# Performance work log

Hardware: AMD Instinct MI355X
Metric: run time of the kernel (lower is better)

## Reference

```python
import jax, jax.numpy as jnp
import numpy as np

IN_FEATURES = 1024
OUT_FEATURES = 64
KERNEL_DIMS = 16
N = 512


def setup_inputs() -> dict:
    key = jax.random.key(0)
    kx, kT = jax.random.split(key)
    x = jax.random.normal(kx, (N, IN_FEATURES), dtype=jnp.float32)
    T = jax.random.normal(kT, (IN_FEATURES, OUT_FEATURES, KERNEL_DIMS), dtype=jnp.float32)
    return {"x": x, "T": T}


def reference(x, T):
    n = x.shape[0]
    # Project: [N, in] @ [in, out*kd] -> [N, out, kd]
    matrices = (x @ T.reshape(T.shape[0], -1)).reshape(n, OUT_FEATURES, KERNEL_DIMS)
    # Pairwise L1 distance over kernel dims: [N, N, out]
    norm = jnp.abs(matrices[None, :, :, :] - matrices[:, None, :, :]).sum(axis=3)
    expnorm = jnp.exp(-norm)
    # Exclude self-similarity (diagonal) and sum over the batch axis
    mask = 1.0 - jnp.eye(n, dtype=x.dtype)
    o_b = (expnorm * mask[:, :, None]).sum(axis=1)  # [N, out]
    return jnp.concatenate([x, o_b], axis=1)
```

## Files before the change

### kernel.cpp

```cpp
#include <hip/hip_runtime.h>
#include <hip/hip_bf16.h>
#include <hip/hip_fp16.h>

#define NB     512
#define INF    1024
#define OUTF   64
#define PROJ   1024
#define OROW   (INF + OUTF)

typedef short short8 __attribute__((ext_vector_type(8)));
typedef float floatx4 __attribute__((ext_vector_type(4)));

#define LDT 40

__device__ __forceinline__ unsigned pack_bf16(float x, float y) {
    __hip_bfloat162 h = __float22bfloat162_rn(make_float2(x, y));
    union { __hip_bfloat162 h; unsigned u; } v; v.h = h; return v.u;
}

__device__ __forceinline__ __half2 as_h2(unsigned u) {
    union { unsigned u; __half2 h; } v; v.u = u; return v.h;
}

__global__ __launch_bounds__(256, 2) void gemm_fused(const float* __restrict__ A,
                                                     const float* __restrict__ B,
                                                     float* __restrict__ out,
                                                     __half* __restrict__ M16) {
    __shared__ short As[16 * LDT];
    __shared__ short Bs[64 * LDT];

    const int t    = threadIdx.x;
    const int lane = t & 63, w = t >> 6;
    const int bnx = blockIdx.x, bmy = blockIdx.y;
    const int bm = bmy * 16, bn = bnx * 64;

    {
        const int r = t >> 4, c4 = (t & 15) * 4;
        *(float4*)&out[(size_t)(bm + r) * OROW + bn + c4] =
            *(const float4*)&A[(size_t)(bm + r) * INF + bn + c4];
    }
    if (t < 16) {
        const int row = bmy * 16 + bnx;
        *(float4*)&out[(size_t)row * OROW + INF + t * 4] =
            make_float4(-1.f, -1.f, -1.f, -1.f);
    }

    const int am = t >> 4,        ak  = (t & 15) * 2;
    const int bk = (t >> 4) * 2,  bn0 = (t & 15) * 4;

    const int q = lane >> 4, c = lane & 15;
    const short* ap = &As[c * LDT + q * 8];
    const short* bp = &Bs[(w * 16 + c) * LDT + q * 8];

    floatx4 acc = {0.f, 0.f, 0.f, 0.f};

    float2 av  = *(const float2*)&A[(size_t)(bm + am) * INF + ak];
    float4 bv0 = *(const float4*)&B[(size_t)bk * PROJ + bn + bn0];
    float4 bv1 = *(const float4*)&B[(size_t)(bk + 1) * PROJ + bn + bn0];

    for (int k0 = 0; k0 < INF; k0 += 32) {
        __syncthreads();
        *(unsigned*)&As[am * LDT + ak]        = pack_bf16(av.x, av.y);
        *(unsigned*)&Bs[(bn0 + 0) * LDT + bk] = pack_bf16(bv0.x, bv1.x);
        *(unsigned*)&Bs[(bn0 + 1) * LDT + bk] = pack_bf16(bv0.y, bv1.y);
        *(unsigned*)&Bs[(bn0 + 2) * LDT + bk] = pack_bf16(bv0.z, bv1.z);
        *(unsigned*)&Bs[(bn0 + 3) * LDT + bk] = pack_bf16(bv0.w, bv1.w);
        __syncthreads();

        const int kn = k0 + 32;
        if (kn < INF) {
            av  = *(const float2*)&A[(size_t)(bm + am) * INF + kn + ak];
            bv0 = *(const float4*)&B[(size_t)(kn + bk) * PROJ + bn + bn0];
            bv1 = *(const float4*)&B[(size_t)(kn + bk + 1) * PROJ + bn + bn0];
        }

        const short8 af = *(const short8*)ap;
        const short8 bf = *(const short8*)bp;
        acc = __builtin_amdgcn_mfma_f32_16x16x32_bf16(af, bf, acc, 0, 0, 0);
    }

#pragma unroll
    for (int r = 0; r < 4; ++r) {
        M16[(size_t)(bm + q * 4 + r) * PROJ + bn + w * 16 + c] = __float2half(acc[r]);
    }
}

__global__ __launch_bounds__(128) void pairwise_h2(const __half* __restrict__ M16,
                                                   float* __restrict__ out) {
    __shared__ __half Mj[64 * 64];

    const int t  = threadIdx.x;
    const int o  = t & 3;
    const int il = t >> 2;
    const int og = blockIdx.x;
    const int ig = blockIdx.y;
    const int j0 = blockIdx.z * 64;
    const int i  = ig * 32 + il;

    const uint4* mp = (const uint4*)&M16[(size_t)i * PROJ + og * 64 + o * 16];
    const uint4 a0 = mp[0], a1 = mp[1];

#pragma unroll
    for (int cc = 0; cc < 4; ++cc) {
        const int idx = (cc * 128 + t) * 8;
        const int jl  = idx >> 6;
        const int col = idx & 63;
        *(uint4*)&Mj[jl * 64 + col] =
            *(const uint4*)&M16[(size_t)(j0 + jl) * PROJ + og * 64 + col];
    }
    __syncthreads();

    float sum0 = 0.f, sum1 = 0.f;
#pragma unroll 4
    for (int jl = 0; jl < 64; ++jl) {
        const uint4 b0 = *(const uint4*)&Mj[jl * 64 + o * 16];
        const uint4 b1 = *(const uint4*)&Mj[jl * 64 + o * 16 + 8];
        __half2 s0 = __hadd2(__habs2(__hsub2(as_h2(a0.x), as_h2(b0.x))),
                             __habs2(__hsub2(as_h2(a0.y), as_h2(b0.y))));
        __half2 s1 = __hadd2(__habs2(__hsub2(as_h2(a0.z), as_h2(b0.z))),
                             __habs2(__hsub2(as_h2(a0.w), as_h2(b0.w))));
        __half2 s2 = __hadd2(__habs2(__hsub2(as_h2(a1.x), as_h2(b1.x))),
                             __habs2(__hsub2(as_h2(a1.y), as_h2(b1.y))));
        __half2 s3 = __hadd2(__habs2(__hsub2(as_h2(a1.z), as_h2(b1.z))),
                             __habs2(__hsub2(as_h2(a1.w), as_h2(b1.w))));
        const __half2 s = __hadd2(__hadd2(s0, s1), __hadd2(s2, s3));
        const float norm = __low2float(s) + __high2float(s);
        if (jl & 1) sum1 += __expf(-norm);
        else        sum0 += __expf(-norm);
    }

    __hip_atomic_fetch_add(&out[(size_t)i * OROW + INF + og * 4 + o],
                           sum0 + sum1, __ATOMIC_RELAXED,
                           __HIP_MEMORY_SCOPE_AGENT);
}

extern "C" void kernel_launch(void* const* d_in, const int* in_sizes, int n_in,
                              void* d_out, int out_size, void* d_ws, size_t ws_size,
                              hipStream_t stream) {
    const float* x = (const float*)d_in[0];
    const float* T = (const float*)d_in[1];
    float* out  = (float*)d_out;
    __half* M16 = (__half*)d_ws;

    gemm_fused<<<dim3(PROJ / 64, NB / 16), 256, 0, stream>>>(x, T, out, M16);
    pairwise_h2<<<dim3(OUTF / 4, NB / 32, NB / 64), 128, 0, stream>>>(M16, out);
}
```

Measured before the change: 92.56 us.

## Double GEMM K-step with k-major B tile and reuse Mj across two rows

The GEMM now stages 64 K values per iteration in a new shared layout (A row-major and B k-pair-major as packed bf16 pairs) and issues two MFMAs per barrier pair. This halves the number of syncthreads and makes the global loads wider. The pairwise kernel gives each thread two i rows, so every Mj tile read from shared memory feeds two L1-distance computations and the grid's y dimension is halved. This raises register use and lowers block count, which could hurt occupancy and latency hiding.

Result: faster. 88.94 us (-3.9%).

```diff
diff --git a/kernel.cpp b/kernel.cpp
--- a/kernel.cpp
+++ b/kernel.cpp
@@ -11,7 +11,8 @@
 typedef short short8 __attribute__((ext_vector_type(8)));
 typedef float floatx4 __attribute__((ext_vector_type(4)));
 
-#define LDT 40
+#define SA 36
+#define SB 68
 
 __device__ __forceinline__ unsigned pack_bf16(float x, float y) {
     __hip_bfloat162 h = __float22bfloat162_rn(make_float2(x, y));
@@ -26,8 +27,8 @@
                                                      const float* __restrict__ B,
                                                      float* __restrict__ out,
                                                      __half* __restrict__ M16) {
-    __shared__ short As[16 * LDT];
-    __shared__ short Bs[64 * LDT];
+    __shared__ unsigned As[16 * SA];
+    __shared__ unsigned Bs[32 * SB];
 
     const int t    = threadIdx.x;
     const int lane = t & 63, w = t >> 6;
@@ -45,44 +46,78 @@
             make_float4(-1.f, -1.f, -1.f, -1.f);
     }
 
-    const int am = t >> 4,        ak  = (t & 15) * 2;
-    const int bk = (t >> 4) * 2,  bn0 = (t & 15) * 4;
+    const int am  = t >> 4;
+    const int ak  = (t & 15) * 4;
+    const int bkp = t >> 4;
+    const int bn0 = (t & 15) * 4;
 
     const int q = lane >> 4, c = lane & 15;
-    const short* ap = &As[c * LDT + q * 8];
-    const short* bp = &Bs[(w * 16 + c) * LDT + q * 8];
+    const unsigned* apo = &As[c * SA + q * 4];
+    const unsigned* bpo = &Bs[(q * 4) * SB + w * 16 + c];
 
     floatx4 acc = {0.f, 0.f, 0.f, 0.f};
 
-    float2 av  = *(const float2*)&A[(size_t)(bm + am) * INF + ak];
-    float4 bv0 = *(const float4*)&B[(size_t)bk * PROJ + bn + bn0];
-    float4 bv1 = *(const float4*)&B[(size_t)(bk + 1) * PROJ + bn + bn0];
+    const size_t aoff  = (size_t)(bm + am) * INF + ak;
+    const float* Bbase = B + bn + bn0;
 
-    for (int k0 = 0; k0 < INF; k0 += 32) {
+    float4 av  = *(const float4*)&A[aoff];
+    float4 b0a = *(const float4*)&Bbase[(size_t)(2 * bkp)      * PROJ];
+    float4 b0b = *(const float4*)&Bbase[(size_t)(2 * bkp + 1)  * PROJ];
+    float4 b1a = *(const float4*)&Bbase[(size_t)(2 * bkp + 32) * PROJ];
+    float4 b1b = *(const float4*)&Bbase[(size_t)(2 * bkp + 33) * PROJ];
+
+    for (int k0 = 0; k0 < INF; k0 += 64) {
         __syncthreads();
-        *(unsigned*)&As[am * LDT + ak]        = pack_bf16(av.x, av.y);
-        *(unsigned*)&Bs[(bn0 + 0) * LDT + bk] = pack_bf16(bv0.x, bv1.x);
-        *(unsigned*)&Bs[(bn0 + 1) * LDT + bk] = pack_bf16(bv0.y, bv1.y);
-        *(unsigned*)&Bs[(bn0 + 2) * LDT + bk] = pack_bf16(bv0.z, bv1.z);
-        *(unsigned*)&Bs[(bn0 + 3) * LDT + bk] = pack_bf16(bv0.w, bv1.w);
+        *(uint2*)&As[am * SA + (ak >> 1)] =
+            make_uint2(pack_bf16(av.x, av.y), pack_bf16(av.z, av.w));
+        *(uint4*)&Bs[bkp * SB + bn0] =
+            make_uint4(pack_bf16(b0a.x, b0b.x), pack_bf16(b0a.y, b0b.y),
+                       pack_bf16(b0a.z, b0b.z), pack_bf16(b0a.w, b0b.w));
+        *(uint4*)&Bs[(bkp + 16) * SB + bn0] =
+            make_uint4(pack_bf16(b1a.x, b1b.x), pack_bf16(b1a.y, b1b.y),
+                       pack_bf16(b1a.z, b1b.z), pack_bf16(b1a.w, b1b.w));
         __syncthreads();
 
-        const int kn = k0 + 32;
+        const int kn = k0 + 64;
         if (kn < INF) {
-            av  = *(const float2*)&A[(size_t)(bm + am) * INF + kn + ak];
-            bv0 = *(const float4*)&B[(size_t)(kn + bk) * PROJ + bn + bn0];
-            bv1 = *(const float4*)&B[(size_t)(kn + bk + 1) * PROJ + bn + bn0];
+            av  = *(const float4*)&A[aoff + kn];
+            b0a = *(const float4*)&Bbase[(size_t)(kn + 2 * bkp)      * PROJ];
+            b0b = *(const float4*)&Bbase[(size_t)(kn + 2 * bkp + 1)  * PROJ];
+            b1a = *(const float4*)&Bbase[(size_t)(kn + 2 * bkp + 32) * PROJ];
+            b1b = *(const float4*)&Bbase[(size_t)(kn + 2 * bkp + 33) * PROJ];
         }
 
-        const short8 af = *(const short8*)ap;
-        const short8 bf = *(const short8*)bp;
-        acc = __builtin_amdgcn_mfma_f32_16x16x32_bf16(af, bf, acc, 0, 0, 0);
+        union { uint4 u; short8 s; } alo, ahi;
+        alo.u = *(const uint4*)(apo);
+        ahi.u = *(const uint4*)(apo + 16);
+        union { unsigned u[4]; short8 s; } blo, bhi;
+#pragma unroll
+        for (int j = 0; j < 4; ++j) {
+            blo.u[j] = bpo[j * SB];
+            bhi.u[j] = bpo[(j + 16) * SB];
+        }
+        acc = __builtin_amdgcn_mfma_f32_16x16x32_bf16(alo.s, blo.s, acc, 0, 0, 0);
+        acc = __builtin_amdgcn_mfma_f32_16x16x32_bf16(ahi.s, bhi.s, acc, 0, 0, 0);
     }
 
 #pragma unroll
     for (int r = 0; r < 4; ++r) {
         M16[(size_t)(bm + q * 4 + r) * PROJ + bn + w * 16 + c] = __float2half(acc[r]);
     }
+}
+
+__device__ __forceinline__ float l1norm16(const uint4 a0, const uint4 a1,
+                                          const uint4 b0, const uint4 b1) {
+    __half2 s0 = __hadd2(__habs2(__hsub2(as_h2(a0.x), as_h2(b0.x))),
+                         __habs2(__hsub2(as_h2(a0.y), as_h2(b0.y))));
+    __half2 s1 = __hadd2(__habs2(__hsub2(as_h2(a0.z), as_h2(b0.z))),
+                         __habs2(__hsub2(as_h2(a0.w), as_h2(b0.w))));
+    __half2 s2 = __hadd2(__habs2(__hsub2(as_h2(a1.x), as_h2(b1.x))),
+                         __habs2(__hsub2(as_h2(a1.y), as_h2(b1.y))));
+    __half2 s3 = __hadd2(__habs2(__hsub2(as_h2(a1.z), as_h2(b1.z))),
+                         __habs2(__hsub2(as_h2(a1.w), as_h2(b1.w))));
+    const __half2 s = __hadd2(__hadd2(s0, s1), __hadd2(s2, s3));
+    return __low2float(s) + __high2float(s);
 }
 
 __global__ __launch_bounds__(128) void pairwise_h2(const __half* __restrict__ M16,
@@ -95,10 +130,13 @@
     const int og = blockIdx.x;
     const int ig = blockIdx.y;
     const int j0 = blockIdx.z * 64;
-    const int i  = ig * 32 + il;
+    const int ia = ig * 64 + il;
+    const int ib = ia + 32;
 
-    const uint4* mp = (const uint4*)&M16[(size_t)i * PROJ + og * 64 + o * 16];
-    const uint4 a0 = mp[0], a1 = mp[1];
+    const uint4* mpa = (const uint4*)&M16[(size_t)ia * PROJ + og * 64 + o * 16];
+    const uint4* mpb = (const uint4*)&M16[(size_t)ib * PROJ + og * 64 + o * 16];
+    const uint4 a0 = mpa[0], a1 = mpa[1];
+    const uint4 a2 = mpb[0], a3 = mpb[1];
 
 #pragma unroll
     for (int cc = 0; cc < 4; ++cc) {
@@ -110,28 +148,21 @@
     }
     __syncthreads();
 
-    float sum0 = 0.f, sum1 = 0.f;
+    float sa0 = 0.f, sa1 = 0.f, sb0 = 0.f, sb1 = 0.f;
 #pragma unroll 4
     for (int jl = 0; jl < 64; ++jl) {
         const uint4 b0 = *(const uint4*)&Mj[jl * 64 + o * 16];
         const uint4 b1 = *(const uint4*)&Mj[jl * 64 + o * 16 + 8];
-        __half2 s0 = __hadd2(__habs2(__hsub2(as_h2(a0.x), as_h2(b0.x))),
-                             __habs2(__hsub2(as_h2(a0.y), as_h2(b0.y))));
-        __half2 s1 = __hadd2(__habs2(__hsub2(as_h2(a0.z), as_h2(b0.z))),
-                             __habs2(__hsub2(as_h2(a0.w), as_h2(b0.w))));
-        __half2 s2 = __hadd2(__habs2(__hsub2(as_h2(a1.x), as_h2(b1.x))),
-                             __habs2(__hsub2(as_h2(a1.y), as_h2(b1.y))));
-        __half2 s3 = __hadd2(__habs2(__hsub2(as_h2(a1.z), as_h2(b1.z))),
-                             __habs2(__hsub2(as_h2(a1.w), as_h2(b1.w))));
-        const __half2 s = __hadd2(__hadd2(s0, s1), __hadd2(s2, s3));
-        const float norm = __low2float(s) + __high2float(s);
-        if (jl & 1) sum1 += __expf(-norm);
-        else        sum0 += __expf(-norm);
+        const float na = l1norm16(a0, a1, b0, b1);
+        const float nb = l1norm16(a2, a3, b0, b1);
+        if (jl & 1) { sa1 += __expf(-na); sb1 += __expf(-nb); }
+        else        { sa0 += __expf(-na); sb0 += __expf(-nb); }
     }
 
-    __hip_atomic_fetch_add(&out[(size_t)i * OROW + INF + og * 4 + o],
-                           sum0 + sum1, __ATOMIC_RELAXED,
-                           __HIP_MEMORY_SCOPE_AGENT);
+    __hip_atomic_fetch_add(&out[(size_t)ia * OROW + INF + og * 4 + o],
+                           sa0 + sa1, __ATOMIC_RELAXED, __HIP_MEMORY_SCOPE_AGENT);
+    __hip_atomic_fetch_add(&out[(size_t)ib * OROW + INF + og * 4 + o],
+                           sb0 + sb1, __ATOMIC_RELAXED, __HIP_MEMORY_SCOPE_AGENT);
 }
 
 extern "C" void kernel_launch(void* const* d_in, const int* in_sizes, int n_in,
@@ -143,5 +174,5 @@
     __half* M16 = (__half*)d_ws;
 
     gemm_fused<<<dim3(PROJ / 64, NB / 16), 256, 0, stream>>>(x, T, out, M16);
-    pairwise_h2<<<dim3(OUTF / 4, NB / 32, NB / 64), 128, 0, stream>>>(M16, out);
+    pairwise_h2<<<dim3(OUTF / 4, NB / 64, NB / 64), 128, 0, stream>>>(M16, out);
 }
```
